# Kernel tuning notes

Measured on AMD Instinct MI355X. Metric: run time of the kernel, lower is better.

## Reference

```python
import math
import jax, jax.numpy as jnp
import numpy as np

B, L, CIN, COUT = 128, 100, 55, 55
D, H, DFF, MODES = 512, 8, 512, 32
E = D // H
KERNELS = (12, 24)
NK = len(KERNELS)


def _pos_emb(length, d):
    pos = np.arange(length)[:, None].astype(np.float32)
    div = np.exp(np.arange(0, d, 2).astype(np.float32) * (-math.log(10000.0) / d))
    pe = np.zeros((length, d), dtype=np.float32)
    pe[:, 0::2] = np.sin(pos * div)
    pe[:, 1::2] = np.cos(pos * div)
    return jnp.asarray(pe)


def _circ_conv3(x, W):
    # Conv1d(kernel=3, padding=1, padding_mode='circular', bias=False); x:(B,L,C) W:(O,C,3)
    n = x.shape[1]
    xp = jnp.concatenate([x[:, -1:], x, x[:, :1]], axis=1)
    return (jnp.einsum('blc,oc->blo', xp[:, 0:n], W[:, :, 0]) +
            jnp.einsum('blc,oc->blo', xp[:, 1:n + 1], W[:, :, 1]) +
            jnp.einsum('blc,oc->blo', xp[:, 2:n + 2], W[:, :, 2]))


def _moving_avg(x, k):
    # replicate-pad then length-preserving mean filter (Autoformer moving_avg)
    front = jnp.repeat(x[:, :1], (k - 1) // 2, axis=1)
    end = jnp.repeat(x[:, -1:], k // 2, axis=1)
    xp = jnp.concatenate([front, x, end], axis=1)
    c = jnp.cumsum(xp, axis=1)
    c = jnp.concatenate([jnp.zeros_like(c[:, :1]), c], axis=1)
    return (c[:, k:] - c[:, :-k]) / float(k)


def _decomp(x, w, b):
    # series_decomp_multi with learned softmax mixing (Linear(1, NK))
    means = jnp.stack([_moving_avg(x, k) for k in KERNELS], axis=-1)  # (B,L,D,NK)
    mix = jax.nn.softmax(x[..., None] * w + b, axis=-1)
    mean = jnp.sum(means * mix, axis=-1)
    return x - mean, mean


def _my_layernorm(x, g, b):
    mu = x.mean(-1, keepdims=True)
    var = ((x - mu) ** 2).mean(-1, keepdims=True)
    xh = (x - mu) / jnp.sqrt(var + 1e-5) * g + b
    return xh - xh.mean(axis=1, keepdims=True)


def _fourier_block(q, Wc):
    # q:(B,L,H,E) -> rfft over L, per-mode complex GEMM with Wc:(H,E,E,MODES), irfft
    x = jnp.transpose(q, (0, 2, 3, 1))  # (B,H,E,L)
    xf = jnp.fft.rfft(x, axis=-1)
    sel = jnp.einsum('bhem,heom->bhom', xf[..., :MODES], Wc)
    nfreq = x.shape[-1] // 2 + 1
    out_ft = jnp.zeros(sel.shape[:-1] + (nfreq,), sel.dtype).at[..., :MODES].set(sel)
    out = jnp.fft.irfft(out_ft, n=x.shape[-1], axis=-1)
    return jnp.transpose(out, (0, 3, 1, 2))  # (B,L,H,E)


def _fourier_cross(q, k, Wc):
    # FourierCrossAttention: frequency-domain q*k attention with tanh activation, values = k
    xq = jnp.transpose(q, (0, 2, 3, 1))
    xk = jnp.transpose(k, (0, 2, 3, 1))
    qf = jnp.fft.rfft(xq, axis=-1)[..., :MODES]
    kf = jnp.fft.rfft(xk, axis=-1)[..., :MODES]
    qk = jnp.tanh(jnp.einsum('bhex,bhey->bhxy', qf, kf))
    qkv = jnp.einsum('bhxy,bhey->bhex', qk, kf)
    w = jnp.einsum('bhex,heox->bhox', qkv, Wc)
    nfreq = xq.shape[-1] // 2 + 1
    out_ft = jnp.zeros(w.shape[:-1] + (nfreq,), w.dtype).at[..., :MODES].set(w)
    out = jnp.fft.irfft(out_ft / float(D * D), n=xq.shape[-1], axis=-1)
    return jnp.transpose(out, (0, 3, 1, 2))


def _heads(x, W, b):
    y = x @ W.T + b
    return y.reshape(y.shape[0], y.shape[1], H, E)


def _gelu(x):
    return jax.nn.gelu(x, approximate=False)


def _forward(x, emb_enc_w, emb_dec_w, enc_proj_w, enc_proj_b, enc_sig_w, enc_sig_b,
             enc_four_wr, enc_four_wi, enc_ffn_w1, enc_ffn_w2, enc_dcmp_w, enc_dcmp_b,
             enc_norm_g, enc_norm_b, dec_proj_w, dec_proj_b, dec_four_wr, dec_four_wi,
             crs_proj_w, crs_proj_b, crs_four_wr, crs_four_wi, dec_ffn_w1, dec_ffn_w2,
             dec_dcmp_w, dec_dcmp_b, dec_trend_w, dec_norm_g, dec_norm_b,
             out_proj_w, out_proj_b):
    b, n, _ = x.shape
    dist = jnp.abs(jnp.arange(n)[:, None] - jnp.arange(n)[None, :]).astype(x.dtype)
    # seasonal-trend init decomposition
    trend_init = jnp.broadcast_to(x.mean(axis=1, keepdims=True), x.shape)
    seasonal_init = x - trend_init
    pe = _pos_emb(n, D)
    enc_four = enc_four_wr + 1j * enc_four_wi
    enc = _circ_conv3(x, emb_enc_w) + pe
    series_l, prior_l, sigma_l = [], [], []
    for i in range(enc_proj_w.shape[0]):  # e_layers (structurally distinct params)
        Wp, bp = enc_proj_w[i], enc_proj_b[i]
        q = _heads(enc, Wp[0], bp[0])
        k = _heads(enc, Wp[1], bp[1])
        v = _heads(enc, Wp[2], bp[2])  # projected but unused by FourierBlock (faithful)
        attn_out = _fourier_block(q, enc_four).reshape(b, n, D) @ Wp[3].T + bp[3]
        # Anomaly-Transformer association: series = softmax(QK^T/sqrt(E)), prior = Gaussian kernel
        scores = jnp.einsum('blhe,bshe->bhls', q, k) / math.sqrt(E)
        series = jax.nn.softmax(scores, axis=-1)
        sig = jnp.transpose(enc @ enc_sig_w[i].T + enc_sig_b[i], (0, 2, 1))  # (B,H,L)
        sig = jnp.power(3.0, jax.nn.sigmoid(5.0 * sig) + 1e-5) - 1.0
        prior = jnp.exp(-dist ** 2 / (2.0 * sig[..., None] ** 2)) / (math.sqrt(2.0 * math.pi) * sig[..., None])
        series_l.append(series); prior_l.append(prior); sigma_l.append(sig)
        h = enc + attn_out
        h, _ = _decomp(h, enc_dcmp_w[i, 0], enc_dcmp_b[i, 0])
        y = _gelu(h @ enc_ffn_w1[i].T) @ enc_ffn_w2[i].T
        enc, _ = _decomp(h + y, enc_dcmp_w[i, 1], enc_dcmp_b[i, 1])
    enc = _my_layernorm(enc, enc_norm_g, enc_norm_b)

    # decoder (d_layers = 1)
    dec = _circ_conv3(seasonal_init, emb_dec_w) + pe
    dec_four = dec_four_wr + 1j * dec_four_wi
    crs_four = crs_four_wr + 1j * crs_four_wi
    q = _heads(dec, dec_proj_w[0], dec_proj_b[0])
    sa = _fourier_block(q, dec_four).reshape(b, n, D) @ dec_proj_w[3].T + dec_proj_b[3]
    h = dec + sa
    h, t1 = _decomp(h, dec_dcmp_w[0], dec_dcmp_b[0])
    qc = _heads(h, crs_proj_w[0], crs_proj_b[0])
    kc = _heads(enc, crs_proj_w[1], crs_proj_b[1])
    ca = _fourier_cross(qc, kc, crs_four).reshape(b, n, D) @ crs_proj_w[3].T + crs_proj_b[3]
    h = h + ca
    h, t2 = _decomp(h, dec_dcmp_w[1], dec_dcmp_b[1])
    y = _gelu(h @ dec_ffn_w1.T) @ dec_ffn_w2.T
    h, t3 = _decomp(h + y, dec_dcmp_w[2], dec_dcmp_b[2])
    residual_trend = _circ_conv3(t1 + t2 + t3, dec_trend_w)  # (B,L,COUT)
    trend = trend_init + residual_trend
    h = _my_layernorm(h, dec_norm_g, dec_norm_b)
    seasonal = h @ out_proj_w.T + out_proj_b
    dec_out = trend + seasonal
    return dec_out, jnp.stack(series_l), jnp.stack(prior_l), jnp.stack(sigma_l)


def setup_inputs() -> dict:
    key = jax.random.key(0)
    ks = iter(jax.random.split(key, 64))

    def rn(shape, s=0.02):
        return s * jax.random.normal(next(ks), shape, dtype=jnp.float32)

    return dict(
        x=jax.random.normal(next(ks), (B, L, CIN), dtype=jnp.float32),
        emb_enc_w=rn((D, CIN, 3)), emb_dec_w=rn((D, CIN, 3)),
        enc_proj_w=rn((2, 4, D, D)), enc_proj_b=jnp.zeros((2, 4, D), jnp.float32),
        enc_sig_w=rn((2, H, D)), enc_sig_b=jnp.zeros((2, H), jnp.float32),
        enc_four_wr=rn((H, E, E, MODES)), enc_four_wi=rn((H, E, E, MODES)),
        enc_ffn_w1=rn((2, DFF, D)), enc_ffn_w2=rn((2, D, DFF)),
        enc_dcmp_w=rn((2, 2, NK), 1.0), enc_dcmp_b=jnp.zeros((2, 2, NK), jnp.float32),
        enc_norm_g=jnp.ones((D,), jnp.float32), enc_norm_b=jnp.zeros((D,), jnp.float32),
        dec_proj_w=rn((4, D, D)), dec_proj_b=jnp.zeros((4, D), jnp.float32),
        dec_four_wr=rn((H, E, E, MODES)), dec_four_wi=rn((H, E, E, MODES)),
        crs_proj_w=rn((4, D, D)), crs_proj_b=jnp.zeros((4, D), jnp.float32),
        crs_four_wr=rn((H, E, E, MODES)), crs_four_wi=rn((H, E, E, MODES)),
        dec_ffn_w1=rn((DFF, D)), dec_ffn_w2=rn((D, DFF)),
        dec_dcmp_w=rn((3, NK), 1.0), dec_dcmp_b=jnp.zeros((3, NK), jnp.float32),
        dec_trend_w=rn((COUT, D, 3)),
        dec_norm_g=jnp.ones((D,), jnp.float32), dec_norm_b=jnp.zeros((D,), jnp.float32),
        out_proj_w=rn((COUT, D)), out_proj_b=jnp.zeros((COUT,), jnp.float32),
    )


def reference(x, emb_enc_w, emb_dec_w, enc_proj_w, enc_proj_b, enc_sig_w, enc_sig_b,
              enc_four_wr, enc_four_wi, enc_ffn_w1, enc_ffn_w2, enc_dcmp_w, enc_dcmp_b,
              enc_norm_g, enc_norm_b, dec_proj_w, dec_proj_b, dec_four_wr, dec_four_wi,
              crs_proj_w, crs_proj_b, crs_four_wr, crs_four_wi, dec_ffn_w1, dec_ffn_w2,
              dec_dcmp_w, dec_dcmp_b, dec_trend_w, dec_norm_g, dec_norm_b,
              out_proj_w, out_proj_b):
    return _forward(x, emb_enc_w, emb_dec_w, enc_proj_w, enc_proj_b, enc_sig_w, enc_sig_b,
                    enc_four_wr, enc_four_wi, enc_ffn_w1, enc_ffn_w2, enc_dcmp_w, enc_dcmp_b,
                    enc_norm_g, enc_norm_b, dec_proj_w, dec_proj_b, dec_four_wr, dec_four_wi,
                    crs_proj_w, crs_proj_b, crs_four_wr, crs_four_wi, dec_ffn_w1, dec_ffn_w2,
                    dec_dcmp_w, dec_dcmp_b, dec_trend_w, dec_norm_g, dec_norm_b,
                    out_proj_w, out_proj_b)
```

## Files before the change

kernel.cpp:

```cpp
#include <hip/hip_runtime.h>
#include <hip/hip_bf16.h>
#include <cmath>

constexpr int B = 128, L = 100, CIN = 55, COUT = 55;
constexpr int D = 512, H = 8, DFF = 512, MODES = 32, E = 64;
constexpr int NK = 2;
constexpr int M_ROWS = B * L;
constexpr int KEMB = 192;
constexpr size_t BLD  = (size_t)B * L * D;
constexpr size_t BHEM = (size_t)B * H * E * MODES;
constexpr size_t BHLL = (size_t)B * H * L * L;
constexpr float INV_SQRT_2PI = 0.3989422804014327f;

static inline int cdiv(int a, int b) { return (a + b - 1) / b; }

typedef short shortx8 __attribute__((ext_vector_type(8)));
typedef float f32x4 __attribute__((ext_vector_type(4)));

__device__ inline unsigned short f2bf(float f)
{
    unsigned int u = __float_as_uint(f);
    unsigned int r = (u + 0x7FFFu + ((u >> 16) & 1u)) >> 16;
    return (unsigned short)r;
}
__device__ inline unsigned short f2bf_n(float f)
{
    union { __hip_bfloat16 h; unsigned short u; } cv;
    cv.h = __float2bfloat16(f);
    return cv.u;
}
__device__ inline float bf2f(unsigned short u)
{
    union { unsigned int i; float f; } c;
    c.i = (unsigned int)u << 16;
    return c.f;
}

__global__ void init_consts(float* __restrict__ pe, float* __restrict__ twc, float* __restrict__ tws)
{
    int idx = blockIdx.x * 256 + threadIdx.x;
    if (idx < L * D) {
        int l = idx / D, d = idx % D;
        int i2 = d & ~1;
        float div = expf((float)i2 * (-logf(10000.f) / (float)D));
        float ang = (float)l * div;
        pe[idx] = (d & 1) ? cosf(ang) : sinf(ang);
    }
    if (idx < L * MODES) {
        int t = idx / MODES, m = idx % MODES;
        float th = 2.f * 3.14159265358979323846f * (float)m * (float)t / (float)L;
        twc[idx] = cosf(th);
        tws[idx] = sinf(th);
    }
}

__global__ void init_tw(unsigned short* __restrict__ twf, unsigned short* __restrict__ twi)
{
    int idx = blockIdx.x * 256 + threadIdx.x;
    if (idx >= 64 * 128) return;
    {
        int mp = idx / 128, t = idx % 128;
        float v = 0.f;
        if (t < L) {
            if (mp < 32) v = cosf(2.f * 3.14159265358979323846f * (float)mp * (float)t / (float)L);
            else v = -sinf(2.f * 3.14159265358979323846f * (float)(mp - 32) * (float)t / (float)L);
        }
        twf[idx] = f2bf(v);
    }
    {
        int t = idx / 64, mp = idx % 64;
        float v = 0.f;
        if (t < L) {
            if (mp == 0) v = 1.f;
            else if (mp < 32) v = 2.f * cosf(2.f * 3.14159265358979323846f * (float)mp * (float)t / (float)L);
            else if (mp == 32) v = 0.f;
            else v = -2.f * sinf(2.f * 3.14159265358979323846f * (float)(mp - 32) * (float)t / (float)L);
        }
        twi[idx] = f2bf(v);
    }
}

__global__ void xmean_kernel(const float* __restrict__ x, float* __restrict__ xm)
{
    int idx = blockIdx.x * 256 + threadIdx.x;
    if (idx >= B * CIN) return;
    int b = idx / CIN, c = idx % CIN;
    float s = 0.f;
    for (int l = 0; l < L; ++l) s += x[((size_t)b * L + l) * CIN + c];
    xm[idx] = s * (1.f / (float)L);
}

__global__ void to_bf16(const float* __restrict__ src, unsigned short* __restrict__ dst, int n4)
{
    int i = blockIdx.x * 256 + threadIdx.x;
    if (i >= n4) return;
    float4 v = *(const float4*)&src[(size_t)i * 4];
    ushort4 h;
    h.x = f2bf(v.x); h.y = f2bf(v.y); h.z = f2bf(v.z); h.w = f2bf(v.w);
    *(ushort4*)&dst[(size_t)i * 4] = h;
}

__global__ void pad_rows_bf(const float* __restrict__ src, unsigned short* __restrict__ dst,
                            int rows_src, int rows_dst, int k_src, int k_dst)
{
    int idx = blockIdx.x * 256 + threadIdx.x;
    if (idx >= rows_dst * k_dst) return;
    int r = idx / k_dst, k = idx % k_dst;
    dst[idx] = (r < rows_src && k < k_src) ? f2bf(src[(size_t)r * k_src + k]) : (unsigned short)0;
}

__global__ void pad_trend_w2_bf(const float* __restrict__ src, unsigned short* __restrict__ dst)
{
    int idx = blockIdx.x * 256 + threadIdx.x;
    if (idx >= 192 * D) return;
    int n = idx / D, d = idx % D;
    int j = n / 64, o = n % 64;
    dst[idx] = (o < COUT) ? f2bf(src[(size_t)o * (D * 3) + d * 3 + j]) : (unsigned short)0;
}

__global__ __launch_bounds__(256) void transpose_w(const float* __restrict__ wr, const float* __restrict__ wi,
                                                   float2* __restrict__ wt)
{
    int h = blockIdx.x / E, e = blockIdx.x % E;
    __shared__ float tr[64][33], ti[64][33];
    for (int i = threadIdx.x; i < E * MODES; i += 256) {
        int o = i / MODES, m = i % MODES;
        size_t s = (((size_t)h * E + e) * E + o) * MODES + m;
        tr[o][m] = wr[s]; ti[o][m] = wi[s];
    }
    __syncthreads();
    for (int i = threadIdx.x; i < MODES * E; i += 256) {
        int m = i / E, o = i % E;
        wt[(((size_t)h * MODES + m) * E + e) * E + o] = make_float2(tr[o][m], ti[o][m]);
    }
}

__global__ void im2col_emb(const float* __restrict__ x, const float* __restrict__ xmean,
                           unsigned short* __restrict__ A2)
{
    int idx = blockIdx.x * 256 + threadIdx.x;
    if (idx >= M_ROWS * KEMB) return;
    int k = idx % KEMB, m = idx / KEMB;
    float v = 0.f;
    if (k < CIN * 3) {
        int c = k / 3, j = k % 3;
        int l = m % L, b = m / L;
        int ls = l + j - 1; ls = (ls + L) % L;
        v = x[((size_t)b * L + ls) * CIN + c];
        if (xmean) v -= xmean[(size_t)b * CIN + c];
    }
    A2[idx] = f2bf(v);
}

template<int BN>
__global__ __launch_bounds__(256) void gemm_mfma(const unsigned short* __restrict__ A,
                                                 const unsigned short* __restrict__ Wb,
                                                 const float* __restrict__ bias, const float* __restrict__ pe,
                                                 float* __restrict__ C, unsigned short* __restrict__ Cb,
                                                 int Nout, int K, int act, int accum)
{
    constexpr int NI = BN / 32;
    constexpr int BI = BN / 64;
    __shared__ unsigned short As[128][40];
    __shared__ unsigned short Bs[BN][40];
    int tid = threadIdx.x;
    int row0 = blockIdx.y * 128, col0 = blockIdx.x * BN;
    int wid = tid >> 6, lane = tid & 63;
    int wm = wid >> 1, wn = wid & 1;
    int lrow = lane & 15, kg = lane >> 4;
    int ar = tid >> 2, ac8 = (tid & 3) * 8;
    f32x4 acc[4][NI] = {};
    shortx8 rah[2], rbh[BI];

    auto loadG = [&](int k0) {
#pragma unroll
        for (int p = 0; p < 2; ++p)
            rah[p] = *(const shortx8*)&A[(size_t)(row0 + p * 64 + ar) * K + k0 + ac8];
#pragma unroll
        for (int p = 0; p < BI; ++p)
            rbh[p] = *(const shortx8*)&Wb[(size_t)(col0 + p * 64 + ar) * K + k0 + ac8];
    };
    auto storeLDS = [&]() {
#pragma unroll
        for (int p = 0; p < 2; ++p)
            *(shortx8*)&As[p * 64 + ar][ac8] = rah[p];
#pragma unroll
        for (int p = 0; p < BI; ++p)
            *(shortx8*)&Bs[p * 64 + ar][ac8] = rbh[p];
    };

    loadG(0);
    for (int k0 = 0; ; ) {
        __syncthreads();
        storeLDS();
        __syncthreads();
        int kn = k0 + 32;
        if (kn < K) loadG(kn);
        shortx8 av[4], bv[NI];
#pragma unroll
        for (int mi = 0; mi < 4; ++mi)
            av[mi] = *(const shortx8*)&As[wm * 64 + mi * 16 + lrow][kg * 8];
#pragma unroll
        for (int ni = 0; ni < NI; ++ni)
            bv[ni] = *(const shortx8*)&Bs[wn * (BN / 2) + ni * 16 + lrow][kg * 8];
#pragma unroll
        for (int mi = 0; mi < 4; ++mi)
#pragma unroll
            for (int ni = 0; ni < NI; ++ni)
                acc[mi][ni] = __builtin_amdgcn_mfma_f32_16x16x32_bf16(av[mi], bv[ni], acc[mi][ni], 0, 0, 0);
        k0 = kn;
        if (k0 >= K) break;
    }
#pragma unroll
    for (int mi = 0; mi < 4; ++mi) {
#pragma unroll
        for (int ni = 0; ni < NI; ++ni) {
            int col = col0 + wn * (BN / 2) + ni * 16 + lrow;
            if (col >= Nout) continue;
#pragma unroll
            for (int r = 0; r < 4; ++r) {
                int row = row0 + wm * 64 + mi * 16 + kg * 4 + r;
                float v = acc[mi][ni][r];
                if (bias) v += bias[col];
                if (pe) v += pe[(size_t)(row % L) * Nout + col];
                if (act) v = 0.5f * v * (1.f + erff(v * 0.70710678118654752f));
                size_t o = (size_t)row * Nout + col;
                if (Cb) Cb[o] = f2bf_n(v);
                else if (accum) C[o] += v;
                else C[o] = v;
            }
        }
    }
}

__global__ __launch_bounds__(256) void scores_softmax(const unsigned short* __restrict__ QK,
                                                      float* __restrict__ out)
{
    int bh = blockIdx.x, b = bh / H, h = bh % H;
    int pass = blockIdx.y;
    __shared__ unsigned short Ks[112][72];
    __shared__ unsigned short Qs[64][72];
    int tid = threadIdx.x;
    int srow = tid >> 4, sc4 = (tid & 15) * 4;
#pragma unroll
    for (int i = 0; i < 7; ++i) {
        int r = i * 16 + srow;
        ushort4 hh = {0, 0, 0, 0};
        if (r < L) hh = *(const ushort4*)&QK[((size_t)b * L + r) * 1024 + 512 + h * E + sc4];
        *(ushort4*)&Ks[r][sc4] = hh;
    }
#pragma unroll
    for (int i = 0; i < 4; ++i) {
        int r = i * 16 + srow;
        int gr = pass * 64 + r;
        ushort4 hh = {0, 0, 0, 0};
        if (gr < L) hh = *(const ushort4*)&QK[((size_t)b * L + gr) * 1024 + h * E + sc4];
        *(ushort4*)&Qs[r][sc4] = hh;
    }
    __syncthreads();
    int wid = tid >> 6, lane = tid & 63;
    int lrow = lane & 15, kg = lane >> 4;
    f32x4 acc[7] = {};
#pragma unroll
    for (int ks = 0; ks < 2; ++ks) {
        shortx8 aq = *(const shortx8*)&Qs[wid * 16 + lrow][ks * 32 + kg * 8];
#pragma unroll
        for (int tj = 0; tj < 7; ++tj) {
            shortx8 bk = *(const shortx8*)&Ks[tj * 16 + lrow][ks * 32 + kg * 8];
            acc[tj] = __builtin_amdgcn_mfma_f32_16x16x32_bf16(aq, bk, acc[tj], 0, 0, 0);
        }
    }
    float mx[4] = {-1e30f, -1e30f, -1e30f, -1e30f};
#pragma unroll
    for (int tj = 0; tj < 7; ++tj) {
        bool valid = (tj * 16 + lrow) < L;
#pragma unroll
        for (int r = 0; r < 4; ++r) {
            float v = acc[tj][r] * 0.125f;
            acc[tj][r] = valid ? v : -1e30f;
            if (valid) mx[r] = fmaxf(mx[r], v);
        }
    }
#pragma unroll
    for (int off = 1; off < 16; off <<= 1)
#pragma unroll
        for (int r = 0; r < 4; ++r) mx[r] = fmaxf(mx[r], __shfl_xor(mx[r], off));
    float sum[4] = {0.f, 0.f, 0.f, 0.f};
#pragma unroll
    for (int tj = 0; tj < 7; ++tj)
#pragma unroll
        for (int r = 0; r < 4; ++r) {
            float e = expf(acc[tj][r] - mx[r]);
            acc[tj][r] = e;
            sum[r] += e;
        }
#pragma unroll
    for (int off = 1; off < 16; off <<= 1)
#pragma unroll
        for (int r = 0; r < 4; ++r) sum[r] += __shfl_xor(sum[r], off);
    float inv[4];
#pragma unroll
    for (int r = 0; r < 4; ++r) inv[r] = 1.f / sum[r];
    float* base = out + (size_t)bh * L * L;
#pragma unroll
    for (int r = 0; r < 4; ++r) {
        int row = pass * 64 + wid * 16 + kg * 4 + r;
        if (row >= L) continue;
#pragma unroll
        for (int tj = 0; tj < 7; ++tj) {
            int col = tj * 16 + lrow;
            if (col < L) base[(size_t)row * L + col] = acc[tj][r] * inv[r];
        }
    }
}

__global__ void trend_combine(const float* __restrict__ Y, const float* __restrict__ xmean,
                              float* __restrict__ dec_out)
{
    int idx = blockIdx.x * 256 + threadIdx.x;
    if (idx >= B * L * COUT) return;
    int o = idx % COUT; int l = (idx / COUT) % L; int b = idx / (COUT * L);
    int lm = (l + L - 1) % L, lp = (l + 1) % L;
    float v = xmean[(size_t)b * CIN + o]
            + Y[((size_t)b * L + lm) * 192 + o]
            + Y[((size_t)b * L + l ) * 192 + 64 + o]
            + Y[((size_t)b * L + lp) * 192 + 128 + o];
    dec_out[idx] = v;
}

__global__ __launch_bounds__(256) void dft_mfma(const unsigned short* __restrict__ X,
                                                const unsigned short* __restrict__ twf,
                                                float2* __restrict__ xf, int stride)
{
    int b = blockIdx.x / H, h = blockIdx.x % H;
    __shared__ unsigned short Xs[64][136];
    int tid = threadIdx.x;
    for (int i = tid; i < L * E / 4; i += 256) {
        int t = i >> 4, e4 = (i & 15) * 4;
        ushort4 u = *(const ushort4*)&X[((size_t)b * L + t) * stride + h * E + e4];
        Xs[e4][t] = u.x; Xs[e4 + 1][t] = u.y; Xs[e4 + 2][t] = u.z; Xs[e4 + 3][t] = u.w;
    }
    for (int i = tid; i < 64 * 28; i += 256) {
        int e = i / 28, t = L + i % 28;
        Xs[e][t] = 0;
    }
    __syncthreads();
    int wid = tid >> 6, lane = tid & 63;
    int lrow = lane & 15, kg = lane >> 4;
    f32x4 acc[4] = {};
#pragma unroll
    for (int k0 = 0; k0 < 4; ++k0) {
        shortx8 bx = *(const shortx8*)&Xs[wid * 16 + lrow][k0 * 32 + kg * 8];
#pragma unroll
        for (int mi = 0; mi < 4; ++mi) {
            shortx8 aw = *(const shortx8*)&twf[(size_t)(mi * 16 + lrow) * 128 + k0 * 32 + kg * 8];
            acc[mi] = __builtin_amdgcn_mfma_f32_16x16x32_bf16(aw, bx, acc[mi], 0, 0, 0);
        }
    }
    int e = wid * 16 + lrow;
#pragma unroll
    for (int mi = 0; mi < 2; ++mi)
#pragma unroll
        for (int r = 0; r < 4; ++r) {
            int m = mi * 16 + kg * 4 + r;
            xf[((size_t)(h * MODES + m) * B + b) * E + e] = make_float2(acc[mi][r], acc[mi + 2][r]);
        }
}

__global__ __launch_bounds__(256) void idft_mfma(const float2* __restrict__ sel,
                                                 const unsigned short* __restrict__ twi,
                                                 unsigned short* __restrict__ out, float scale)
{
    int b = blockIdx.x / H, h = blockIdx.x % H;
    __shared__ unsigned short Ss[64][72];
    int tid = threadIdx.x;
    for (int i = tid; i < MODES * E; i += 256) {
        int m = i >> 6, o = i & 63;
        float2 v = sel[((size_t)(h * MODES + m) * B + b) * E + o];
        Ss[o][m] = f2bf_n(v.x);
        Ss[o][m + 32] = f2bf_n(v.y);
    }
    __syncthreads();
    int wid = tid >> 6, lane = tid & 63;
    int lrow = lane & 15, kg = lane >> 4;
    f32x4 acc[2][4] = {};
#pragma unroll
    for (int k0 = 0; k0 < 2; ++k0) {
        shortx8 bs[4];
#pragma unroll
        for (int ni = 0; ni < 4; ++ni)
            bs[ni] = *(const shortx8*)&Ss[ni * 16 + lrow][k0 * 32 + kg * 8];
#pragma unroll
        for (int ti = 0; ti < 2; ++ti) {
            shortx8 at = *(const shortx8*)&twi[(size_t)((wid * 2 + ti) * 16 + lrow) * 64 + k0 * 32 + kg * 8];
#pragma unroll
            for (int ni = 0; ni < 4; ++ni)
                acc[ti][ni] = __builtin_amdgcn_mfma_f32_16x16x32_bf16(at, bs[ni], acc[ti][ni], 0, 0, 0);
        }
    }
#pragma unroll
    for (int ti = 0; ti < 2; ++ti)
#pragma unroll
        for (int ni = 0; ni < 4; ++ni)
#pragma unroll
            for (int r = 0; r < 4; ++r) {
                int t = (wid * 2 + ti) * 16 + kg * 4 + r;
                if (t < L) {
                    int o = ni * 16 + lrow;
                    out[((size_t)b * L + t) * D + h * E + o] = f2bf_n(acc[ti][ni][r] * scale);
                }
            }
}

__global__ __launch_bounds__(256) void mode_gemm2(float2* __restrict__ xf, const float2* __restrict__ wt)
{
    int hm = blockIdx.x;
    int bt = blockIdx.y;
    __shared__ float2 Wc[E][E];
    __shared__ float2 Ac[32][E];
    for (int i = threadIdx.x; i < E * E; i += 256) Wc[i / E][i % E] = wt[(size_t)hm * (E * E) + i];
    for (int i = threadIdx.x; i < 32 * E; i += 256)
        Ac[i / E][i % E] = xf[((size_t)hm * B + bt * 32 + i / E) * E + i % E];
    __syncthreads();
    int o = threadIdx.x & 63, bb = threadIdx.x >> 6;
    float2 acc[8];
#pragma unroll
    for (int j = 0; j < 8; ++j) acc[j] = make_float2(0.f, 0.f);
    for (int e = 0; e < E; ++e) {
        float2 w = Wc[e][o];
#pragma unroll
        for (int j = 0; j < 8; ++j) {
            float2 a = Ac[bb * 8 + j][e];
            acc[j].x += a.x * w.x - a.y * w.y;
            acc[j].y += a.x * w.y + a.y * w.x;
        }
    }
#pragma unroll
    for (int j = 0; j < 8; ++j)
        xf[((size_t)hm * B + bt * 32 + bb * 8 + j) * E + o] = acc[j];
}

__global__ __launch_bounds__(256) void fourier_qk(const float2* __restrict__ qf, float2* __restrict__ kf)
{
    int b = blockIdx.x / H, h = blockIdx.x % H;
    __shared__ float2 qm[MODES][E + 1], km[MODES][E + 1], vm[MODES][E + 1];
    __shared__ float tr[MODES][MODES + 1], ti[MODES][MODES + 1];
    for (int i = threadIdx.x; i < MODES * E; i += 256) {
        int m = i / E, e = i % E;
        size_t idx = ((size_t)(h * MODES + m) * B + b) * E + e;
        qm[m][e] = qf[idx];
        km[m][e] = kf[idx];
    }
    __syncthreads();
    for (int i = threadIdx.x; i < MODES * MODES; i += 256) {
        int x = i / MODES, y = i % MODES;
        float re = 0.f, im = 0.f;
        for (int e = 0; e < E; ++e) {
            float2 a = qm[x][e], k2 = km[y][e];
            re += a.x * k2.x - a.y * k2.y;
            im += a.x * k2.y + a.y * k2.x;
        }
        float aa = fminf(fmaxf(2.f * re, -30.f), 30.f);
        float b2 = 2.f * im;
        float den = coshf(aa) + cosf(b2);
        tr[x][y] = sinhf(aa) / den;
        ti[x][y] = sinf(b2) / den;
    }
    __syncthreads();
    for (int i = threadIdx.x; i < MODES * E; i += 256) {
        int x = i / E, e = i % E;
        float re = 0.f, im = 0.f;
        for (int y = 0; y < MODES; ++y) {
            float ar = tr[x][y], ai = ti[x][y];
            float2 kk = km[y][e];
            re += ar * kk.x - ai * kk.y;
            im += ar * kk.y + ai * kk.x;
        }
        vm[x][e] = make_float2(re, im);
    }
    __syncthreads();
    for (int i = threadIdx.x; i < MODES * E; i += 256) {
        int m = i / E, e = i % E;
        kf[((size_t)(h * MODES + m) * B + b) * E + e] = vm[m][e];
    }
}

__global__ __launch_bounds__(256) void sigma_kernel(const unsigned short* __restrict__ enc,
                                                    const float* __restrict__ w,
                                                    const float* __restrict__ bias, float* __restrict__ sig_out)
{
    __shared__ float wsh[H][D];
    for (int i = threadIdx.x; i < H * D; i += 256) wsh[i / D][i % D] = w[i];
    __syncthreads();
    int wid = threadIdx.x / 64, lane = threadIdx.x % 64;
    int row = blockIdx.x * 4 + wid;
    const unsigned short* p = enc + (size_t)row * D;
    float xv[8];
#pragma unroll
    for (int i = 0; i < 8; ++i) xv[i] = bf2f(p[lane + i * 64]);
    int b = row / L, l = row % L;
#pragma unroll
    for (int h = 0; h < H; ++h) {
        float s = 0.f;
#pragma unroll
        for (int i = 0; i < 8; ++i) s += xv[i] * wsh[h][lane + i * 64];
        for (int off = 32; off; off >>= 1) s += __shfl_xor(s, off);
        if (lane == 0) {
            float acc = s + bias[h];
            float sg = 1.f / (1.f + expf(-5.f * acc));
            float val = expf((sg + 1e-5f) * 1.0986122886681098f) - 1.f;
            sig_out[((size_t)b * H + h) * L + l] = val;
        }
    }
}

__global__ void prior_kernel(const float* __restrict__ sig, float* __restrict__ prior)
{
    int idx = blockIdx.x * 256 + threadIdx.x;
    if (idx >= (int)(B * H * L * L)) return;
    int s = idx % L; int l = (idx / L) % L; int bh = idx / (L * L);
    float sg = sig[(size_t)bh * L + l];
    float d = (float)abs(l - s);
    prior[idx] = expf(-d * d / (2.f * sg * sg)) * INV_SQRT_2PI / sg;
}

__global__ __launch_bounds__(256) void decomp_kernel(const unsigned short* __restrict__ in1,
                                                     const unsigned short* __restrict__ in2,
                                                     const float* __restrict__ w, const float* __restrict__ bc,
                                                     unsigned short* __restrict__ res, float* __restrict__ trend,
                                                     int tmode)
{
    int b = blockIdx.x / (D / 64);
    int d0 = (blockIdx.x % (D / 64)) * 64;
    __shared__ float P[125][65];
    __shared__ float qtot[4][64];
    int tid = threadIdx.x;
    int dd = tid & 63, q = tid >> 6;
    int p0 = q * 31;
    float run = 0.f;
#pragma unroll
    for (int i = 0; i < 31; ++i) {
        int p = p0 + i;
        int j = min(max(p - 12, 0), L - 1);
        size_t g = ((size_t)b * L + j) * D + d0 + dd;
        float v = bf2f(in1[g]);
        if (in2) v += bf2f(in2[g]);
        run += v;
        P[p + 1][dd] = run;
    }
    qtot[q][dd] = run;
    if (tid < 64) P[0][dd] = 0.f;
    __syncthreads();
    if (q > 0) {
        float off = qtot[0][dd];
        if (q > 1) off += qtot[1][dd];
        if (q > 2) off += qtot[2][dd];
#pragma unroll
        for (int i = 0; i < 31; ++i)
            P[p0 + i + 1][dd] += off;
    }
    __syncthreads();
    float w0 = w[0], w1 = w[1], b0 = bc[0], b1 = bc[1];
    for (int i = tid; i < L * 64; i += 256) {
        int l = i >> 6, d2 = i & 63;
        float s12 = P[l + 19][d2] - P[l + 7][d2];
        float s24 = P[l + 25][d2] - P[l + 1][d2];
        float x = P[l + 13][d2] - P[l + 12][d2];
        float m0 = s12 * (1.f / 12.f), m1 = s24 * (1.f / 24.f);
        float z0 = x * w0 + b0, z1 = x * w1 + b1;
        float zm = fmaxf(z0, z1);
        float e0 = expf(z0 - zm), e1 = expf(z1 - zm);
        float p0f = e0 / (e0 + e1);
        float mean = m0 * p0f + m1 * (1.f - p0f);
        size_t g = ((size_t)b * L + l) * D + d0 + d2;
        res[g] = f2bf_n(x - mean);
        if (tmode == 1) trend[g] = mean;
        else if (tmode == 2) trend[g] += mean;
    }
}

__global__ __launch_bounds__(256) void ln_row(const unsigned short* __restrict__ x, const float* __restrict__ g,
                                              const float* __restrict__ bb, float* __restrict__ out)
{
    int row = blockIdx.x;
    const unsigned short* p = x + (size_t)row * D;
    float s = 0.f, s2 = 0.f;
    for (int d = threadIdx.x; d < D; d += 256) { float v = bf2f(p[d]); s += v; s2 += v * v; }
    for (int off = 32; off; off >>= 1) { s += __shfl_xor(s, off); s2 += __shfl_xor(s2, off); }
    __shared__ float red[8];
    int wid = threadIdx.x / 64, lane = threadIdx.x % 64;
    if (lane == 0) { red[wid] = s; red[4 + wid] = s2; }
    __syncthreads();
    if (threadIdx.x == 0) {
        red[0] = red[0] + red[1] + red[2] + red[3];
        red[4] = red[4] + red[5] + red[6] + red[7];
    }
    __syncthreads();
    float mu = red[0] / (float)D;
    float var = red[4] / (float)D - mu * mu;
    float rstd = rsqrtf(var + 1e-5f);
    for (int d = threadIdx.x; d < D; d += 256)
        out[(size_t)row * D + d] = (bf2f(p[d]) - mu) * rstd * g[d] + bb[d];
}

__global__ __launch_bounds__(256) void col_sub(const float* __restrict__ xh, unsigned short* __restrict__ out)
{
    int b = blockIdx.x / (D / 128);
    int d0 = (blockIdx.x % (D / 128)) * 128;
    int c = threadIdx.x & 127, half = threadIdx.x >> 7;
    __shared__ float red[2][128];
    float s = 0.f;
    for (int l = half * 50; l < half * 50 + 50; ++l)
        s += xh[((size_t)b * L + l) * D + d0 + c];
    red[half][c] = s;
    __syncthreads();
    float mean = (red[0][c] + red[1][c]) * (1.f / (float)L);
    for (int l = half * 50; l < half * 50 + 50; ++l) {
        size_t g = ((size_t)b * L + l) * D + d0 + c;
        out[g] = f2bf_n(xh[g] - mean);
    }
}

extern "C" void kernel_launch(void* const* d_in, const int* in_sizes, int n_in,
                              void* d_out, int out_size, void* d_ws, size_t ws_size,
                              hipStream_t stream)
{
    const float* x           = (const float*)d_in[0];
    const float* emb_enc_w   = (const float*)d_in[1];
    const float* emb_dec_w   = (const float*)d_in[2];
    const float* enc_proj_w  = (const float*)d_in[3];
    const float* enc_proj_b  = (const float*)d_in[4];
    const float* enc_sig_w   = (const float*)d_in[5];
    const float* enc_sig_b   = (const float*)d_in[6];
    const float* enc_four_wr = (const float*)d_in[7];
    const float* enc_four_wi = (const float*)d_in[8];
    const float* enc_ffn_w1  = (const float*)d_in[9];
    const float* enc_ffn_w2  = (const float*)d_in[10];
    const float* enc_dcmp_w  = (const float*)d_in[11];
    const float* enc_dcmp_b  = (const float*)d_in[12];
    const float* enc_norm_g  = (const float*)d_in[13];
    const float* enc_norm_b  = (const float*)d_in[14];
    const float* dec_proj_w  = (const float*)d_in[15];
    const float* dec_proj_b  = (const float*)d_in[16];
    const float* dec_four_wr = (const float*)d_in[17];
    const float* dec_four_wi = (const float*)d_in[18];
    const float* crs_proj_w  = (const float*)d_in[19];
    const float* crs_proj_b  = (const float*)d_in[20];
    const float* crs_four_wr = (const float*)d_in[21];
    const float* crs_four_wi = (const float*)d_in[22];
    const float* dec_ffn_w1  = (const float*)d_in[23];
    const float* dec_ffn_w2  = (const float*)d_in[24];
    const float* dec_dcmp_w  = (const float*)d_in[25];
    const float* dec_dcmp_b  = (const float*)d_in[26];
    const float* dec_trend_w = (const float*)d_in[27];
    const float* dec_norm_g  = (const float*)d_in[28];
    const float* dec_norm_b  = (const float*)d_in[29];
    const float* out_proj_w  = (const float*)d_in[30];
    const float* out_proj_b  = (const float*)d_in[31];

    float* ws = (float*)d_ws;
    size_t off = 0;
    float* pe    = ws + off; off += (size_t)L * D;
    float* twc   = ws + off; off += (size_t)L * MODES;
    float* tws_  = ws + off; off += (size_t)L * MODES;
    float* xmean = ws + off; off += (size_t)B * CIN;
    float* bufF  = ws + off; off += BLD;
    float* tacc  = ws + off; off += BLD;
    float2* xfc  = (float2*)(ws + off); off += 2 * BHEM;
    float2* kfc  = (float2*)(ws + off); off += 2 * BHEM;
    float2* wtb  = (float2*)(ws + off); off += 2 * (size_t)H * MODES * E * E;
    unsigned short* qk16 = (unsigned short*)(ws + off); off += BLD;
    unsigned short* e16  = (unsigned short*)(ws + off); off += BLD / 2;
    unsigned short* c16  = (unsigned short*)(ws + off); off += BLD / 2;
    unsigned short* d16  = (unsigned short*)(ws + off); off += BLD / 2;
    unsigned short* h16  = (unsigned short*)(ws + off); off += BLD / 2;
    unsigned short* t16  = (unsigned short*)(ws + off); off += BLD / 2;
    unsigned short* im16 = (unsigned short*)(ws + off); off += (size_t)M_ROWS * KEMB / 2;
    unsigned short* wbf_encproj = (unsigned short*)(ws + off); off += (size_t)2 * 4 * D * D / 2;
    unsigned short* wbf_ffn1    = (unsigned short*)(ws + off); off += (size_t)2 * DFF * D / 2;
    unsigned short* wbf_ffn2    = (unsigned short*)(ws + off); off += (size_t)2 * D * DFF / 2;
    unsigned short* wbf_decproj = (unsigned short*)(ws + off); off += (size_t)4 * D * D / 2;
    unsigned short* wbf_crsproj = (unsigned short*)(ws + off); off += (size_t)4 * D * D / 2;
    unsigned short* wbf_dffn1   = (unsigned short*)(ws + off); off += (size_t)DFF * D / 2;
    unsigned short* wbf_dffn2   = (unsigned short*)(ws + off); off += (size_t)D * DFF / 2;
    unsigned short* wbf_embenc  = (unsigned short*)(ws + off); off += (size_t)D * KEMB / 2;
    unsigned short* wbf_embdec  = (unsigned short*)(ws + off); off += (size_t)D * KEMB / 2;
    unsigned short* wbf_trd     = (unsigned short*)(ws + off); off += (size_t)192 * D / 2;
    unsigned short* wbf_seas    = (unsigned short*)(ws + off); off += (size_t)64 * D / 2;
    unsigned short* twf         = (unsigned short*)(ws + off); off += (size_t)64 * 128 / 2;
    unsigned short* twi         = (unsigned short*)(ws + off); off += (size_t)128 * 64 / 2;
    unsigned short* a16 = qk16;
    unsigned short* b16 = qk16 + BLD;

    float* out       = (float*)d_out;
    float* dec_out   = out;
    float* series_out= out + (size_t)B * L * COUT;
    float* prior_out = series_out + 2 * BHLL;
    float* sigma_out = prior_out + 2 * BHLL;

    const int BH = B * H;

    init_consts<<<200, 256, 0, stream>>>(pe, twc, tws_);
    init_tw<<<32, 256, 0, stream>>>(twf, twi);
    xmean_kernel<<<cdiv(B * CIN, 256), 256, 0, stream>>>(x, xmean);
    to_bf16<<<cdiv(2 * 4 * D * D / 4, 256), 256, 0, stream>>>(enc_proj_w, wbf_encproj, 2 * 4 * D * D / 4);
    to_bf16<<<cdiv(2 * DFF * D / 4, 256), 256, 0, stream>>>(enc_ffn_w1, wbf_ffn1, 2 * DFF * D / 4);
    to_bf16<<<cdiv(2 * D * DFF / 4, 256), 256, 0, stream>>>(enc_ffn_w2, wbf_ffn2, 2 * D * DFF / 4);
    to_bf16<<<cdiv(4 * D * D / 4, 256), 256, 0, stream>>>(dec_proj_w, wbf_decproj, 4 * D * D / 4);
    to_bf16<<<cdiv(4 * D * D / 4, 256), 256, 0, stream>>>(crs_proj_w, wbf_crsproj, 4 * D * D / 4);
    to_bf16<<<cdiv(DFF * D / 4, 256), 256, 0, stream>>>(dec_ffn_w1, wbf_dffn1, DFF * D / 4);
    to_bf16<<<cdiv(D * DFF / 4, 256), 256, 0, stream>>>(dec_ffn_w2, wbf_dffn2, D * DFF / 4);
    pad_rows_bf<<<cdiv(D * KEMB, 256), 256, 0, stream>>>(emb_enc_w, wbf_embenc, D, D, CIN * 3, KEMB);
    pad_rows_bf<<<cdiv(D * KEMB, 256), 256, 0, stream>>>(emb_dec_w, wbf_embdec, D, D, CIN * 3, KEMB);
    pad_trend_w2_bf<<<cdiv(192 * D, 256), 256, 0, stream>>>(dec_trend_w, wbf_trd);
    pad_rows_bf<<<cdiv(64 * D, 256), 256, 0, stream>>>(out_proj_w, wbf_seas, COUT, 64, D, D);
    transpose_w<<<H * E, 256, 0, stream>>>(enc_four_wr, enc_four_wi, wtb);

    auto gemm = [&](const unsigned short* A, const unsigned short* Wb, const float* bias, const float* pe_,
                    float* C, unsigned short* Cb, int N, int Nout, int K, int act, int accum) {
        if (N % 128 == 0) {
            dim3 grid(N / 128, M_ROWS / 128);
            gemm_mfma<128><<<grid, 256, 0, stream>>>(A, Wb, bias, pe_, C, Cb, Nout, K, act, accum);
        } else {
            dim3 grid(N / 64, M_ROWS / 128);
            gemm_mfma<64><<<grid, 256, 0, stream>>>(A, Wb, bias, pe_, C, Cb, Nout, K, act, accum);
        }
    };
    dim3 mg_grid(H * MODES, B / 32);
    dim3 sc_grid(BH, 2);

    im2col_emb<<<cdiv(M_ROWS * KEMB, 256), 256, 0, stream>>>(x, nullptr, im16);
    gemm(im16, wbf_embenc, nullptr, pe, nullptr, e16, D, D, KEMB, 0, 0);

    for (int i = 0; i < 2; ++i) {
        const unsigned short* Wp = wbf_encproj + (size_t)i * 4 * D * D;
        const float* bp = enc_proj_b + (size_t)i * 4 * D;
        float* series_i = series_out + (size_t)i * BHLL;
        float* prior_i  = prior_out  + (size_t)i * BHLL;
        float* sigma_i  = sigma_out  + (size_t)i * B * H * L;

        gemm(e16, Wp, bp, nullptr, nullptr, qk16, 1024, 1024, D, 0, 0);
        dft_mfma<<<BH, 256, 0, stream>>>(qk16, twf, xfc, 1024);
        mode_gemm2<<<mg_grid, 256, 0, stream>>>(xfc, wtb);
        idft_mfma<<<BH, 256, 0, stream>>>(xfc, twi, c16, 1.f / (float)L);
        gemm(c16, Wp + (size_t)3 * D * D, bp + 3 * D, nullptr, nullptr, d16, D, D, D, 0, 0);
        scores_softmax<<<sc_grid, 256, 0, stream>>>(qk16, series_i);
        sigma_kernel<<<M_ROWS / 4, 256, 0, stream>>>(e16, enc_sig_w + (size_t)i * H * D,
                                                     enc_sig_b + (size_t)i * H, sigma_i);
        prior_kernel<<<cdiv((int)BHLL, 256), 256, 0, stream>>>(sigma_i, prior_i);
        decomp_kernel<<<B * (D / 64), 256, 0, stream>>>(e16, d16, enc_dcmp_w + (size_t)(i * 2 + 0) * NK,
                                                        enc_dcmp_b + (size_t)(i * 2 + 0) * NK, h16, nullptr, 0);
        gemm(h16, wbf_ffn1 + (size_t)i * DFF * D, nullptr, nullptr, nullptr, c16, DFF, DFF, D, 1, 0);
        gemm(c16, wbf_ffn2 + (size_t)i * D * DFF, nullptr, nullptr, nullptr, d16, D, D, DFF, 0, 0);
        decomp_kernel<<<B * (D / 64), 256, 0, stream>>>(h16, d16, enc_dcmp_w + (size_t)(i * 2 + 1) * NK,
                                                        enc_dcmp_b + (size_t)(i * 2 + 1) * NK, e16, nullptr, 0);
    }
    ln_row<<<M_ROWS, 256, 0, stream>>>(e16, enc_norm_g, enc_norm_b, bufF);
    col_sub<<<B * (D / 128), 256, 0, stream>>>(bufF, e16);

    transpose_w<<<H * E, 256, 0, stream>>>(dec_four_wr, dec_four_wi, wtb);
    im2col_emb<<<cdiv(M_ROWS * KEMB, 256), 256, 0, stream>>>(x, xmean, im16);
    gemm(im16, wbf_embdec, nullptr, pe, nullptr, a16, D, D, KEMB, 0, 0);
    gemm(a16, wbf_decproj, dec_proj_b, nullptr, nullptr, b16, D, D, D, 0, 0);
    dft_mfma<<<BH, 256, 0, stream>>>(b16, twf, xfc, D);
    mode_gemm2<<<mg_grid, 256, 0, stream>>>(xfc, wtb);
    idft_mfma<<<BH, 256, 0, stream>>>(xfc, twi, c16, 1.f / (float)L);
    gemm(c16, wbf_decproj + (size_t)3 * D * D, dec_proj_b + 3 * D, nullptr, nullptr, d16, D, D, D, 0, 0);
    decomp_kernel<<<B * (D / 64), 256, 0, stream>>>(a16, d16, dec_dcmp_w, dec_dcmp_b, h16, tacc, 1);

    gemm(h16, wbf_crsproj, crs_proj_b, nullptr, nullptr, b16, D, D, D, 0, 0);
    dft_mfma<<<BH, 256, 0, stream>>>(b16, twf, xfc, D);
    gemm(e16, wbf_crsproj + (size_t)D * D, crs_proj_b + D, nullptr, nullptr, b16, D, D, D, 0, 0);
    dft_mfma<<<BH, 256, 0, stream>>>(b16, twf, kfc, D);
    transpose_w<<<H * E, 256, 0, stream>>>(crs_four_wr, crs_four_wi, wtb);
    fourier_qk<<<BH, 256, 0, stream>>>(xfc, kfc);
    mode_gemm2<<<mg_grid, 256, 0, stream>>>(kfc, wtb);
    idft_mfma<<<BH, 256, 0, stream>>>(kfc, twi, c16, 1.f / ((float)L * (float)D * (float)D));
    gemm(c16, wbf_crsproj + (size_t)3 * D * D, crs_proj_b + 3 * D, nullptr, nullptr, d16, D, D, D, 0, 0);
    decomp_kernel<<<B * (D / 64), 256, 0, stream>>>(h16, d16, dec_dcmp_w + NK, dec_dcmp_b + NK, a16, tacc, 2);

    gemm(a16, wbf_dffn1, nullptr, nullptr, nullptr, c16, DFF, DFF, D, 1, 0);
    gemm(c16, wbf_dffn2, nullptr, nullptr, nullptr, d16, D, D, DFF, 0, 0);
    decomp_kernel<<<B * (D / 64), 256, 0, stream>>>(a16, d16, dec_dcmp_w + 2 * NK, dec_dcmp_b + 2 * NK, b16, tacc, 2);

    to_bf16<<<cdiv((int)(BLD / 4), 256), 256, 0, stream>>>(tacc, t16, (int)(BLD / 4));
    gemm(t16, wbf_trd, nullptr, nullptr, bufF, nullptr, 192, 192, D, 0, 0);
    trend_combine<<<cdiv(B * L * COUT, 256), 256, 0, stream>>>(bufF, xmean, dec_out);

    ln_row<<<M_ROWS, 256, 0, stream>>>(b16, dec_norm_g, dec_norm_b, bufF);
    col_sub<<<B * (D / 128), 256, 0, stream>>>(bufF, d16);
    gemm(d16, wbf_seas, out_proj_b, nullptr, dec_out, nullptr, 64, COUT, D, 0, 1);
}
```

Baseline: 1.328 ms.

## Double-buffer GEMM LDS and fuse sigma/prior, layernorm/colsub, trend conversion

```diff
diff --git a/kernel.cpp b/kernel.cpp
--- a/kernel.cpp
+++ b/kernel.cpp
@@ -36,7 +36,7 @@
     return c.f;
 }
 
-__global__ void init_consts(float* __restrict__ pe, float* __restrict__ twc, float* __restrict__ tws)
+__global__ void init_consts(float* __restrict__ pe)
 {
     int idx = blockIdx.x * 256 + threadIdx.x;
     if (idx < L * D) {
@@ -45,12 +45,6 @@
         float div = expf((float)i2 * (-logf(10000.f) / (float)D));
         float ang = (float)l * div;
         pe[idx] = (d & 1) ? cosf(ang) : sinf(ang);
-    }
-    if (idx < L * MODES) {
-        int t = idx / MODES, m = idx % MODES;
-        float th = 2.f * 3.14159265358979323846f * (float)m * (float)t / (float)L;
-        twc[idx] = cosf(th);
-        tws[idx] = sinf(th);
     }
 }
 
@@ -161,8 +155,8 @@
 {
     constexpr int NI = BN / 32;
     constexpr int BI = BN / 64;
-    __shared__ unsigned short As[128][40];
-    __shared__ unsigned short Bs[BN][40];
+    __shared__ unsigned short As[2][128][40];
+    __shared__ unsigned short Bs[2][BN][40];
     int tid = threadIdx.x;
     int row0 = blockIdx.y * 128, col0 = blockIdx.x * BN;
     int wid = tid >> 6, lane = tid & 63;
@@ -180,36 +174,40 @@
         for (int p = 0; p < BI; ++p)
             rbh[p] = *(const shortx8*)&Wb[(size_t)(col0 + p * 64 + ar) * K + k0 + ac8];
     };
-    auto storeLDS = [&]() {
+    auto storeLDS = [&](int buf) {
 #pragma unroll
         for (int p = 0; p < 2; ++p)
-            *(shortx8*)&As[p * 64 + ar][ac8] = rah[p];
+            *(shortx8*)&As[buf][p * 64 + ar][ac8] = rah[p];
 #pragma unroll
         for (int p = 0; p < BI; ++p)
-            *(shortx8*)&Bs[p * 64 + ar][ac8] = rbh[p];
+            *(shortx8*)&Bs[buf][p * 64 + ar][ac8] = rbh[p];
     };
 
+    int nk = K >> 5;
     loadG(0);
-    for (int k0 = 0; ; ) {
-        __syncthreads();
-        storeLDS();
-        __syncthreads();
-        int kn = k0 + 32;
-        if (kn < K) loadG(kn);
+    storeLDS(0);
+    if (nk > 1) loadG(32);
+    __syncthreads();
+    int cur = 0;
+    for (int s = 0; s < nk; ++s) {
+        if (s + 1 < nk) {
+            storeLDS(cur ^ 1);
+            if (s + 2 < nk) loadG((s + 2) << 5);
+        }
         shortx8 av[4], bv[NI];
 #pragma unroll
         for (int mi = 0; mi < 4; ++mi)
-            av[mi] = *(const shortx8*)&As[wm * 64 + mi * 16 + lrow][kg * 8];
+            av[mi] = *(const shortx8*)&As[cur][wm * 64 + mi * 16 + lrow][kg * 8];
 #pragma unroll
         for (int ni = 0; ni < NI; ++ni)
-            bv[ni] = *(const shortx8*)&Bs[wn * (BN / 2) + ni * 16 + lrow][kg * 8];
+            bv[ni] = *(const shortx8*)&Bs[cur][wn * (BN / 2) + ni * 16 + lrow][kg * 8];
 #pragma unroll
         for (int mi = 0; mi < 4; ++mi)
 #pragma unroll
             for (int ni = 0; ni < NI; ++ni)
                 acc[mi][ni] = __builtin_amdgcn_mfma_f32_16x16x32_bf16(av[mi], bv[ni], acc[mi][ni], 0, 0, 0);
-        k0 = kn;
-        if (k0 >= K) break;
+        if (s + 1 < nk) __syncthreads();
+        cur ^= 1;
     }
 #pragma unroll
     for (int mi = 0; mi < 4; ++mi) {
@@ -485,9 +483,10 @@
     }
 }
 
-__global__ __launch_bounds__(256) void sigma_kernel(const unsigned short* __restrict__ enc,
-                                                    const float* __restrict__ w,
-                                                    const float* __restrict__ bias, float* __restrict__ sig_out)
+__global__ __launch_bounds__(256) void sigma_prior(const unsigned short* __restrict__ enc,
+                                                   const float* __restrict__ w,
+                                                   const float* __restrict__ bias,
+                                                   float* __restrict__ sig_out, float* __restrict__ prior)
 {
     __shared__ float wsh[H][D];
     for (int i = threadIdx.x; i < H * D; i += 256) wsh[i / D][i % D] = w[i];
@@ -505,30 +504,25 @@
 #pragma unroll
         for (int i = 0; i < 8; ++i) s += xv[i] * wsh[h][lane + i * 64];
         for (int off = 32; off; off >>= 1) s += __shfl_xor(s, off);
-        if (lane == 0) {
-            float acc = s + bias[h];
-            float sg = 1.f / (1.f + expf(-5.f * acc));
-            float val = expf((sg + 1e-5f) * 1.0986122886681098f) - 1.f;
-            sig_out[((size_t)b * H + h) * L + l] = val;
-        }
-    }
-}
-
-__global__ void prior_kernel(const float* __restrict__ sig, float* __restrict__ prior)
-{
-    int idx = blockIdx.x * 256 + threadIdx.x;
-    if (idx >= (int)(B * H * L * L)) return;
-    int s = idx % L; int l = (idx / L) % L; int bh = idx / (L * L);
-    float sg = sig[(size_t)bh * L + l];
-    float d = (float)abs(l - s);
-    prior[idx] = expf(-d * d / (2.f * sg * sg)) * INV_SQRT_2PI / sg;
+        float acc = s + bias[h];
+        float sg = 1.f / (1.f + expf(-5.f * acc));
+        float val = expf((sg + 1e-5f) * 1.0986122886681098f) - 1.f;
+        if (lane == 0) sig_out[((size_t)b * H + h) * L + l] = val;
+        float inv2 = 1.f / (2.f * val * val);
+        float coef = INV_SQRT_2PI / val;
+        float* pr = prior + (((size_t)b * H + h) * L + l) * L;
+        for (int sc = lane; sc < L; sc += 64) {
+            float d = (float)abs(l - sc);
+            pr[sc] = expf(-d * d * inv2) * coef;
+        }
+    }
 }
 
 __global__ __launch_bounds__(256) void decomp_kernel(const unsigned short* __restrict__ in1,
                                                      const unsigned short* __restrict__ in2,
                                                      const float* __restrict__ w, const float* __restrict__ bc,
                                                      unsigned short* __restrict__ res, float* __restrict__ trend,
-                                                     int tmode)
+                                                     unsigned short* __restrict__ trend16, int tmode)
 {
     int b = blockIdx.x / (D / 64);
     int d0 = (blockIdx.x % (D / 64)) * 64;
@@ -575,49 +569,58 @@
         size_t g = ((size_t)b * L + l) * D + d0 + d2;
         res[g] = f2bf_n(x - mean);
         if (tmode == 1) trend[g] = mean;
-        else if (tmode == 2) trend[g] += mean;
-    }
-}
-
-__global__ __launch_bounds__(256) void ln_row(const unsigned short* __restrict__ x, const float* __restrict__ g,
-                                              const float* __restrict__ bb, float* __restrict__ out)
-{
-    int row = blockIdx.x;
-    const unsigned short* p = x + (size_t)row * D;
-    float s = 0.f, s2 = 0.f;
-    for (int d = threadIdx.x; d < D; d += 256) { float v = bf2f(p[d]); s += v; s2 += v * v; }
-    for (int off = 32; off; off >>= 1) { s += __shfl_xor(s, off); s2 += __shfl_xor(s2, off); }
-    __shared__ float red[8];
-    int wid = threadIdx.x / 64, lane = threadIdx.x % 64;
-    if (lane == 0) { red[wid] = s; red[4 + wid] = s2; }
-    __syncthreads();
-    if (threadIdx.x == 0) {
-        red[0] = red[0] + red[1] + red[2] + red[3];
-        red[4] = red[4] + red[5] + red[6] + red[7];
-    }
-    __syncthreads();
-    float mu = red[0] / (float)D;
-    float var = red[4] / (float)D - mu * mu;
-    float rstd = rsqrtf(var + 1e-5f);
-    for (int d = threadIdx.x; d < D; d += 256)
-        out[(size_t)row * D + d] = (bf2f(p[d]) - mu) * rstd * g[d] + bb[d];
-}
-
-__global__ __launch_bounds__(256) void col_sub(const float* __restrict__ xh, unsigned short* __restrict__ out)
-{
-    int b = blockIdx.x / (D / 128);
-    int d0 = (blockIdx.x % (D / 128)) * 128;
-    int c = threadIdx.x & 127, half = threadIdx.x >> 7;
-    __shared__ float red[2][128];
-    float s = 0.f;
-    for (int l = half * 50; l < half * 50 + 50; ++l)
-        s += xh[((size_t)b * L + l) * D + d0 + c];
-    red[half][c] = s;
-    __syncthreads();
-    float mean = (red[0][c] + red[1][c]) * (1.f / (float)L);
-    for (int l = half * 50; l < half * 50 + 50; ++l) {
-        size_t g = ((size_t)b * L + l) * D + d0 + c;
-        out[g] = f2bf_n(xh[g] - mean);
+        else if (tmode == 2) {
+            float tv = trend[g] + mean;
+            trend[g] = tv;
+            if (trend16) trend16[g] = f2bf_n(tv);
+        }
+    }
+}
+
+__global__ __launch_bounds__(256) void ln_colsub(const unsigned short* __restrict__ x,
+                                                 const float* __restrict__ g, const float* __restrict__ bb,
+                                                 unsigned short* __restrict__ out)
+{
+    int b = blockIdx.x;
+    __shared__ unsigned short xs[L][D];
+    __shared__ float colmean[D];
+    __shared__ float gs[D], bs2[D];
+    int tid = threadIdx.x;
+    for (int i = tid; i < L * D / 8; i += 256) {
+        int l = i / 64, c8 = (i % 64) * 8;
+        *(shortx8*)&xs[l][c8] = *(const shortx8*)&x[((size_t)b * L + l) * D + c8];
+    }
+    for (int i = tid; i < D; i += 256) { gs[i] = g[i]; bs2[i] = bb[i]; }
+    __syncthreads();
+    int wid = tid >> 6, lane = tid & 63;
+    for (int l = wid; l < L; l += 4) {
+        float v[8];
+        float s = 0.f, s2 = 0.f;
+#pragma unroll
+        for (int i = 0; i < 8; ++i) {
+            v[i] = bf2f(xs[l][lane + i * 64]);
+            s += v[i]; s2 += v[i] * v[i];
+        }
+        for (int off = 32; off; off >>= 1) { s += __shfl_xor(s, off); s2 += __shfl_xor(s2, off); }
+        float mu = s / (float)D;
+        float var = s2 / (float)D - mu * mu;
+        float rstd = rsqrtf(var + 1e-5f);
+#pragma unroll
+        for (int i = 0; i < 8; ++i) {
+            int d = lane + i * 64;
+            xs[l][d] = f2bf_n((v[i] - mu) * rstd * gs[d] + bs2[d]);
+        }
+    }
+    __syncthreads();
+    for (int c = tid; c < D; c += 256) {
+        float s = 0.f;
+        for (int l = 0; l < L; ++l) s += bf2f(xs[l][c]);
+        colmean[c] = s * (1.f / (float)L);
+    }
+    __syncthreads();
+    for (int i = tid; i < L * D; i += 256) {
+        int l = i / D, c = i % D;
+        out[((size_t)b * L + l) * D + c] = f2bf_n(bf2f(xs[l][c]) - colmean[c]);
     }
 }
 
@@ -661,8 +664,6 @@
     float* ws = (float*)d_ws;
     size_t off = 0;
     float* pe    = ws + off; off += (size_t)L * D;
-    float* twc   = ws + off; off += (size_t)L * MODES;
-    float* tws_  = ws + off; off += (size_t)L * MODES;
     float* xmean = ws + off; off += (size_t)B * CIN;
     float* bufF  = ws + off; off += BLD;
     float* tacc  = ws + off; off += BLD;
@@ -700,7 +701,7 @@
 
     const int BH = B * H;
 
-    init_consts<<<200, 256, 0, stream>>>(pe, twc, tws_);
+    init_consts<<<200, 256, 0, stream>>>(pe);
     init_tw<<<32, 256, 0, stream>>>(twf, twi);
     xmean_kernel<<<cdiv(B * CIN, 256), 256, 0, stream>>>(x, xmean);
     to_bf16<<<cdiv(2 * 4 * D * D / 4, 256), 256, 0, stream>>>(enc_proj_w, wbf_encproj, 2 * 4 * D * D / 4);
@@ -745,18 +746,16 @@
         idft_mfma<<<BH, 256, 0, stream>>>(xfc, twi, c16, 1.f / (float)L);
         gemm(c16, Wp + (size_t)3 * D * D, bp + 3 * D, nullptr, nullptr, d16, D, D, D, 0, 0);
         scores_softmax<<<sc_grid, 256, 0, stream>>>(qk16, series_i);
-        sigma_kernel<<<M_ROWS / 4, 256, 0, stream>>>(e16, enc_sig_w + (size_t)i * H * D,
-                                                     enc_sig_b + (size_t)i * H, sigma_i);
-        prior_kernel<<<cdiv((int)BHLL, 256), 256, 0, stream>>>(sigma_i, prior_i);
+        sigma_prior<<<M_ROWS / 4, 256, 0, stream>>>(e16, enc_sig_w + (size_t)i * H * D,
+                                                    enc_sig_b + (size_t)i * H, sigma_i, prior_i);
         decomp_kernel<<<B * (D / 64), 256, 0, stream>>>(e16, d16, enc_dcmp_w + (size_t)(i * 2 + 0) * NK,
-                                                        enc_dcmp_b + (size_t)(i * 2 + 0) * NK, h16, nullptr, 0);
+                                                        enc_dcmp_b + (size_t)(i * 2 + 0) * NK, h16, nullptr, nullptr, 0);
         gemm(h16, wbf_ffn1 + (size_t)i * DFF * D, nullptr, nullptr, nullptr, c16, DFF, DFF, D, 1, 0);
         gemm(c16, wbf_ffn2 + (size_t)i * D * DFF, nullptr, nullptr, nullptr, d16, D, D, DFF, 0, 0);
         decomp_kernel<<<B * (D / 64), 256, 0, stream>>>(h16, d16, enc_dcmp_w + (size_t)(i * 2 + 1) * NK,
-                                                        enc_dcmp_b + (size_t)(i * 2 + 1) * NK, e16, nullptr, 0);
-    }
-    ln_row<<<M_ROWS, 256, 0, stream>>>(e16, enc_norm_g, enc_norm_b, bufF);
-    col_sub<<<B * (D / 128), 256, 0, stream>>>(bufF, e16);
+                                                        enc_dcmp_b + (size_t)(i * 2 + 1) * NK, e16, nullptr, nullptr, 0);
+    }
+    ln_colsub<<<B, 256, 0, stream>>>(e16, enc_norm_g, enc_norm_b, e16);
 
     transpose_w<<<H * E, 256, 0, stream>>>(dec_four_wr, dec_four_wi, wtb);
     im2col_emb<<<cdiv(M_ROWS * KEMB, 256), 256, 0, stream>>>(x, xmean, im16);
@@ -766,7 +765,7 @@
     mode_gemm2<<<mg_grid, 256, 0, stream>>>(xfc, wtb);
     idft_mfma<<<BH, 256, 0, stream>>>(xfc, twi, c16, 1.f / (float)L);
     gemm(c16, wbf_decproj + (size_t)3 * D * D, dec_proj_b + 3 * D, nullptr, nullptr, d16, D, D, D, 0, 0);
-    decomp_kernel<<<B * (D / 64), 256, 0, stream>>>(a16, d16, dec_dcmp_w, dec_dcmp_b, h16, tacc, 1);
+    decomp_kernel<<<B * (D / 64), 256, 0, stream>>>(a16, d16, dec_dcmp_w, dec_dcmp_b, h16, tacc, nullptr, 1);
 
     gemm(h16, wbf_crsproj, crs_proj_b, nullptr, nullptr, b16, D, D, D, 0, 0);
     dft_mfma<<<BH, 256, 0, stream>>>(b16, twf, xfc, D);
@@ -777,17 +776,15 @@
     mode_gemm2<<<mg_grid, 256, 0, stream>>>(kfc, wtb);
     idft_mfma<<<BH, 256, 0, stream>>>(kfc, twi, c16, 1.f / ((float)L * (float)D * (float)D));
     gemm(c16, wbf_crsproj + (size_t)3 * D * D, crs_proj_b + 3 * D, nullptr, nullptr, d16, D, D, D, 0, 0);
-    decomp_kernel<<<B * (D / 64), 256, 0, stream>>>(h16, d16, dec_dcmp_w + NK, dec_dcmp_b + NK, a16, tacc, 2);
+    decomp_kernel<<<B * (D / 64), 256, 0, stream>>>(h16, d16, dec_dcmp_w + NK, dec_dcmp_b + NK, a16, tacc, nullptr, 2);
 
     gemm(a16, wbf_dffn1, nullptr, nullptr, nullptr, c16, DFF, DFF, D, 1, 0);
     gemm(c16, wbf_dffn2, nullptr, nullptr, nullptr, d16, D, D, DFF, 0, 0);
-    decomp_kernel<<<B * (D / 64), 256, 0, stream>>>(a16, d16, dec_dcmp_w + 2 * NK, dec_dcmp_b + 2 * NK, b16, tacc, 2);
-
-    to_bf16<<<cdiv((int)(BLD / 4), 256), 256, 0, stream>>>(tacc, t16, (int)(BLD / 4));
+    decomp_kernel<<<B * (D / 64), 256, 0, stream>>>(a16, d16, dec_dcmp_w + 2 * NK, dec_dcmp_b + 2 * NK, b16, tacc, t16, 2);
+
     gemm(t16, wbf_trd, nullptr, nullptr, bufF, nullptr, 192, 192, D, 0, 0);
     trend_combine<<<cdiv(B * L * COUT, 256), 256, 0, stream>>>(bufF, xmean, dec_out);
 
-    ln_row<<<M_ROWS, 256, 0, stream>>>(b16, dec_norm_g, dec_norm_b, bufF);
-    col_sub<<<B * (D / 128), 256, 0, stream>>>(bufF, d16);
+    ln_colsub<<<B, 256, 0, stream>>>(b16, dec_norm_g, dec_norm_b, d16);
     gemm(d16, wbf_seas, out_proj_b, nullptr, dec_out, nullptr, 64, COUT, D, 0, 1);
 }
```

After: 1.303 ms. About the same (-1.9%).
